# Optimization experiments

Measured on AMD Instinct MI355X. Metric: run time of the kernel, lower is better.

## Reference

```python
import jax, jax.numpy as jnp
import numpy as np
from jax import lax

B, IN_CH, OUT_CH, H, W_SP, K, PAD = 4, 64, 128, 56, 56, 3, 1


def setup_inputs() -> dict:
    key = jax.random.key(0)
    k1, k2, k3 = jax.random.split(key, 3)
    x = jax.random.normal(k1, (B, IN_CH, H, W_SP), dtype=jnp.float32)
    W = jax.random.normal(k2, (OUT_CH, IN_CH, K, K), dtype=jnp.float32) * 0.05
    b = jax.random.normal(k3, (OUT_CH,), dtype=jnp.float32) * 0.05
    return {"x": x, "W": W, "b": b}


def reference(x, W, b):
    in_ch, out_ch = W.shape[1], W.shape[0]
    # make_preadd_conv: grouped (depthwise-expanded) conv with groups=in_ch.
    # Permuted kernel order: preadd channel p = i*out_ch + j uses kernel W[j, i].
    rhs = jnp.transpose(W, (1, 0, 2, 3)).reshape(in_ch * out_ch, 1, K, K)  # OIHW
    preadd = lax.conv_general_dilated(
        x, rhs,
        window_strides=(1, 1),
        padding=((PAD, PAD), (PAD, PAD)),
        feature_group_count=in_ch,
        dimension_numbers=("NCHW", "OIHW", "NCHW"),
    )  # [B, in_ch*out_ch, H, W]
    bsz, _, h, w = preadd.shape
    # permute_add_featuremaps: out channel o = sum_i preadd[:, i*out_ch + o]
    added = preadd.reshape(bsz, in_ch, out_ch, h, w).sum(axis=1)
    return added + b[:, None, None]
```

## Files before the change

kernel.cpp:

```cpp
#include <hip/hip_runtime.h>
#include <hip/hip_bf16.h>

#define BATCH 4
#define IC 64
#define OC 128
#define HSZ 56
#define WSZ 56
#define HW 3136
#define KTOT 576
#define PTILE 64
#define HALO 57
#define XROWS 178

typedef __attribute__((ext_vector_type(8))) short bf16x8;
typedef __attribute__((ext_vector_type(4))) float f32x4;

__global__ __launch_bounds__(256) void wcvt_kernel(const float* __restrict__ W,
                                                   unsigned short* __restrict__ Wb) {
    int idx = blockIdx.x * 256 + threadIdx.x;
    if (idx >= OC * KTOT) return;
    int o = idx / KTOT;
    int k = idx - o * KTOT;
    int tap = k >> 6;
    int ch = k & 63;
    float v = W[(o * IC + ch) * 9 + tap];
    __hip_bfloat16 h = __float2bfloat16(v);
    Wb[idx] = *reinterpret_cast<unsigned short*>(&h);
}

__global__ __launch_bounds__(512) void conv_mfma_kernel(
    const float* __restrict__ x,
    const unsigned short* __restrict__ Wb,
    const float* __restrict__ bias,
    float* __restrict__ out)
{
    __shared__ unsigned short xs[XROWS * 64];

    const int tid = threadIdx.x;
    const int b  = blockIdx.y;
    const int p0 = blockIdx.x * PTILE;

    const float* xb = x + (size_t)b * IC * HW;

    for (int it = 0; it < 23; ++it) {
        int idx = it * 512 + tid;
        if (idx < XROWS * IC) {
            int ch  = idx / XROWS;
            int pix = idx - ch * XROWS;
            int gp  = p0 - HALO + pix;
            gp = min(max(gp, 0), HW - 1);
            float v = xb[ch * HW + gp];
            __hip_bfloat16 h = __float2bfloat16(v);
            int chunk = (ch >> 3) ^ (pix & 7);
            xs[pix * 64 + chunk * 8 + (ch & 7)] = *reinterpret_cast<unsigned short*>(&h);
        }
    }
    __syncthreads();

    const int lane = tid & 63;
    const int wid  = tid >> 6;
    const int pg   = wid & 3;
    const int og   = wid >> 2;
    const int lrow = lane & 15;
    const int lk   = lane >> 4;

    const int tpix = pg * 16 + lrow;
    const int apix = p0 + tpix;
    const int ah = apix / WSZ;
    const int aw = apix - ah * WSZ;

    unsigned vmask = 0;
#pragma unroll
    for (int t = 0; t < 9; ++t) {
        int hh = ah + (t / 3) - 1;
        int ww = aw + (t % 3) - 1;
        if ((unsigned)hh < (unsigned)HSZ && (unsigned)ww < (unsigned)WSZ)
            vmask |= (1u << t);
    }

    const unsigned short* wb = Wb + (size_t)(og * 64 + lrow) * KTOT + 8 * lk;

    f32x4 acc[4] = {{0,0,0,0},{0,0,0,0},{0,0,0,0},{0,0,0,0}};
    const bf16x8 zfrag = {0,0,0,0,0,0,0,0};

#pragma unroll 3
    for (int tap = 0; tap < 9; ++tap) {
        const int row = tpix + (tap / 3) * WSZ + (tap % 3);
        const bool valid = (vmask >> tap) & 1u;
        const int rbase = row * 64;
        const int rsw = row & 7;
#pragma unroll
        for (int half = 0; half < 2; ++half) {
            const int chunk = (4 * half + lk) ^ rsw;
            bf16x8 a = *reinterpret_cast<const bf16x8*>(&xs[rbase + chunk * 8]);
            a = valid ? a : zfrag;
            const unsigned short* wp = wb + tap * 64 + half * 32;
            bf16x8 b0 = *reinterpret_cast<const bf16x8*>(wp);
            bf16x8 b1 = *reinterpret_cast<const bf16x8*>(wp + 16 * KTOT);
            bf16x8 b2 = *reinterpret_cast<const bf16x8*>(wp + 32 * KTOT);
            bf16x8 b3 = *reinterpret_cast<const bf16x8*>(wp + 48 * KTOT);
            acc[0] = __builtin_amdgcn_mfma_f32_16x16x32_bf16(a, b0, acc[0], 0, 0, 0);
            acc[1] = __builtin_amdgcn_mfma_f32_16x16x32_bf16(a, b1, acc[1], 0, 0, 0);
            acc[2] = __builtin_amdgcn_mfma_f32_16x16x32_bf16(a, b2, acc[2], 0, 0, 0);
            acc[3] = __builtin_amdgcn_mfma_f32_16x16x32_bf16(a, b3, acc[3], 0, 0, 0);
        }
    }

    const int pstore = p0 + pg * 16 + 4 * lk;
#pragma unroll
    for (int bg = 0; bg < 4; ++bg) {
        const int o = og * 64 + bg * 16 + lrow;
        f32x4 r = acc[bg] + bias[o];
        *reinterpret_cast<f32x4*>(&out[((size_t)(b * OC + o)) * HW + pstore]) = r;
    }
}

extern "C" void kernel_launch(void* const* d_in, const int* in_sizes, int n_in,
                              void* d_out, int out_size, void* d_ws, size_t ws_size,
                              hipStream_t stream) {
    const float* x    = (const float*)d_in[0];
    const float* W    = (const float*)d_in[1];
    const float* bias = (const float*)d_in[2];
    float* out        = (float*)d_out;
    unsigned short* Wb = (unsigned short*)d_ws;

    wcvt_kernel<<<(OC * KTOT + 255) / 256, 256, 0, stream>>>(W, Wb);
    dim3 grid(HW / PTILE, BATCH, 1);
    conv_mfma_kernel<<<grid, 512, 0, stream>>>(x, Wb, bias, out);
}
```

Baseline: 31.71 us.

## Pre-transpose input to channel-last bf16 in prep kernel, drop LDS staging

A combined prep kernel now converts both the weights and the input x into bf16. The input is stored in a pixel-major, channel-contiguous layout with zero guard rows. The conv kernel then reads A fragments directly from global memory instead of staging a per-block halo tile in LDS. The grid also splits output channels across blocks (256 threads, 2 oc groups), so the per-block x conversion is no longer duplicated with halo overhead. In exchange this adds an extra global write and read of the bf16 input and relies on L2/cache hits for the repeated tap loads.

Result: slower. 32.57 us (+2.7%).

```diff
diff --git a/kernel.cpp b/kernel.cpp
--- a/kernel.cpp
+++ b/kernel.cpp
@@ -8,93 +8,99 @@
 #define WSZ 56
 #define HW 3136
 #define KTOT 576
-#define PTILE 64
-#define HALO 57
-#define XROWS 178
+#define GUARD 64
+#define XPIX (HW + 2*GUARD)
 
 typedef __attribute__((ext_vector_type(8))) short bf16x8;
 typedef __attribute__((ext_vector_type(4))) float f32x4;
 
-__global__ __launch_bounds__(256) void wcvt_kernel(const float* __restrict__ W,
-                                                   unsigned short* __restrict__ Wb) {
-    int idx = blockIdx.x * 256 + threadIdx.x;
-    if (idx >= OC * KTOT) return;
-    int o = idx / KTOT;
-    int k = idx - o * KTOT;
-    int tap = k >> 6;
-    int ch = k & 63;
-    float v = W[(o * IC + ch) * 9 + tap];
-    __hip_bfloat16 h = __float2bfloat16(v);
-    Wb[idx] = *reinterpret_cast<unsigned short*>(&h);
+__global__ __launch_bounds__(256) void prep_kernel(
+    const float* __restrict__ x,
+    const float* __restrict__ W,
+    unsigned short* __restrict__ Wb,
+    unsigned short* __restrict__ xbf)
+{
+    const int blk = blockIdx.x;
+    const int t   = threadIdx.x;
+
+    if (blk < BATCH * 51) {
+        const int b    = blk / 51;
+        const int tile = blk - b * 51;
+        const int px   = (t & 63);
+        const int chg  = t >> 6;
+        const int gp   = tile * 64 - GUARD + px;
+        const bool inb = (unsigned)gp < (unsigned)HW;
+        const float* xb = x + (size_t)b * IC * HW;
+
+        unsigned short __attribute__((aligned(16))) v[16];
+#pragma unroll
+        for (int i = 0; i < 16; ++i) {
+            const int ch = chg * 16 + i;
+            float f = inb ? xb[ch * HW + gp] : 0.0f;
+            __hip_bfloat16 h = __float2bfloat16(f);
+            v[i] = *reinterpret_cast<unsigned short*>(&h);
+        }
+        unsigned short* dst = xbf + ((size_t)b * XPIX + (gp + GUARD)) * IC + chg * 16;
+        *reinterpret_cast<uint4*>(dst)     = *reinterpret_cast<uint4*>(&v[0]);
+        *reinterpret_cast<uint4*>(dst + 8) = *reinterpret_cast<uint4*>(&v[8]);
+    } else {
+        const int j = (blk - BATCH * 51) * 256 + t;
+        if (j < OC * KTOT) {
+            const int o   = j / KTOT;
+            const int k   = j - o * KTOT;
+            const int tap = k >> 6;
+            const int ch  = k & 63;
+            __hip_bfloat16 h = __float2bfloat16(W[(o * IC + ch) * 9 + tap]);
+            Wb[j] = *reinterpret_cast<unsigned short*>(&h);
+        }
+    }
 }
 
-__global__ __launch_bounds__(512) void conv_mfma_kernel(
-    const float* __restrict__ x,
+__global__ __launch_bounds__(256) void conv_mfma_kernel(
+    const unsigned short* __restrict__ xbf,
     const unsigned short* __restrict__ Wb,
     const float* __restrict__ bias,
     float* __restrict__ out)
 {
-    __shared__ unsigned short xs[XROWS * 64];
-
-    const int tid = threadIdx.x;
-    const int b  = blockIdx.y;
-    const int p0 = blockIdx.x * PTILE;
-
-    const float* xb = x + (size_t)b * IC * HW;
-
-    for (int it = 0; it < 23; ++it) {
-        int idx = it * 512 + tid;
-        if (idx < XROWS * IC) {
-            int ch  = idx / XROWS;
-            int pix = idx - ch * XROWS;
-            int gp  = p0 - HALO + pix;
-            gp = min(max(gp, 0), HW - 1);
-            float v = xb[ch * HW + gp];
-            __hip_bfloat16 h = __float2bfloat16(v);
-            int chunk = (ch >> 3) ^ (pix & 7);
-            xs[pix * 64 + chunk * 8 + (ch & 7)] = *reinterpret_cast<unsigned short*>(&h);
-        }
-    }
-    __syncthreads();
-
-    const int lane = tid & 63;
-    const int wid  = tid >> 6;
-    const int pg   = wid & 3;
-    const int og   = wid >> 2;
+    const int t    = threadIdx.x;
+    const int lane = t & 63;
+    const int pg   = t >> 6;
     const int lrow = lane & 15;
     const int lk   = lane >> 4;
 
-    const int tpix = pg * 16 + lrow;
-    const int apix = p0 + tpix;
+    const int p0 = blockIdx.x * 64;
+    const int og = blockIdx.y;
+    const int b  = blockIdx.z;
+
+    const int apix = p0 + pg * 16 + lrow;
     const int ah = apix / WSZ;
     const int aw = apix - ah * WSZ;
 
     unsigned vmask = 0;
 #pragma unroll
-    for (int t = 0; t < 9; ++t) {
-        int hh = ah + (t / 3) - 1;
-        int ww = aw + (t % 3) - 1;
+    for (int tp = 0; tp < 9; ++tp) {
+        const int hh = ah + (tp / 3) - 1;
+        const int ww = aw + (tp % 3) - 1;
         if ((unsigned)hh < (unsigned)HSZ && (unsigned)ww < (unsigned)WSZ)
-            vmask |= (1u << t);
+            vmask |= (1u << tp);
     }
 
-    const unsigned short* wb = Wb + (size_t)(og * 64 + lrow) * KTOT + 8 * lk;
+    const unsigned short* xa = xbf + ((size_t)b * XPIX + GUARD + apix) * IC + lk * 8;
+    const unsigned short* wb = Wb + (size_t)(og * 64 + lrow) * KTOT + lk * 8;
 
     f32x4 acc[4] = {{0,0,0,0},{0,0,0,0},{0,0,0,0},{0,0,0,0}};
     const bf16x8 zfrag = {0,0,0,0,0,0,0,0};
 
-#pragma unroll 3
-    for (int tap = 0; tap < 9; ++tap) {
-        const int row = tpix + (tap / 3) * WSZ + (tap % 3);
-        const bool valid = (vmask >> tap) & 1u;
-        const int rbase = row * 64;
-        const int rsw = row & 7;
+#pragma unroll
+    for (int tp = 0; tp < 9; ++tp) {
+        const int toff = ((tp / 3) - 1) * WSZ + ((tp % 3) - 1);
+        const bool valid = (vmask >> tp) & 1u;
+        const unsigned short* xrow = xa + toff * IC;
 #pragma unroll
         for (int half = 0; half < 2; ++half) {
-            const int chunk = (4 * half + lk) ^ rsw;
-            bf16x8 a = *reinterpret_cast<const bf16x8*>(&xs[rbase + chunk * 8]);
+            bf16x8 a = *reinterpret_cast<const bf16x8*>(xrow + half * 32);
             a = valid ? a : zfrag;
-            const unsigned short* wp = wb + tap * 64 + half * 32;
+            const unsigned short* wp = wb + tp * 64 + half * 32;
             bf16x8 b0 = *reinterpret_cast<const bf16x8*>(wp);
             bf16x8 b1 = *reinterpret_cast<const bf16x8*>(wp + 16 * KTOT);
             bf16x8 b2 = *reinterpret_cast<const bf16x8*>(wp + 32 * KTOT);
@@ -122,9 +128,13 @@
     const float* W    = (const float*)d_in[1];
     const float* bias = (const float*)d_in[2];
     float* out        = (float*)d_out;
-    unsigned short* Wb = (unsigned short*)d_ws;
 
-    wcvt_kernel<<<(OC * KTOT + 255) / 256, 256, 0, stream>>>(W, Wb);
-    dim3 grid(HW / PTILE, BATCH, 1);
-    conv_mfma_kernel<<<grid, 512, 0, stream>>>(x, Wb, bias, out);
+    unsigned short* Wb  = (unsigned short*)d_ws;
+    unsigned short* xbf = (unsigned short*)((char*)d_ws + 147456);
+
+    const int wblocks = (OC * KTOT + 255) / 256;
+    prep_kernel<<<BATCH * 51 + wblocks, 256, 0, stream>>>(x, W, Wb, xbf);
+
+    dim3 grid(HW / 64, 2, BATCH);
+    conv_mfma_kernel<<<grid, 256, 0, stream>>>(xbf, Wb, bias, out);
 }
```
